# Kernel tuning notes

Hardware: AMD Instinct MI355X
Metric: run time of the kernel (lower is better)

Reference implementation:

```python
import jax, jax.numpy as jnp
import numpy as np

D_MODEL = 1024
N_HEADS = 16
D_K = D_MODEL // N_HEADS  # 64
THETA = 10000.0
MAX_SEQ_LEN = 2048


def _rope_cache():
    k = jnp.arange(D_K // 2, dtype=jnp.float32)
    inv_freq = THETA ** (-2.0 * k / D_K)  # [P]
    pos = jnp.arange(MAX_SEQ_LEN, dtype=jnp.float32)
    angles = pos[:, None] * inv_freq[None, :]  # [max_seq_len, P]
    return jnp.cos(angles), jnp.sin(angles)


def _apply_rope(x, cos, sin):
    # x: [B, H, S, d_k]; cos/sin: [B, 1, S, d_k//2] (broadcast over heads)
    x_even = x[..., 0::2]
    x_odd = x[..., 1::2]
    r_even = x_even * cos - x_odd * sin
    r_odd = x_even * sin + x_odd * cos
    # re-interleave pairs: [..., P, 2] -> [..., d_k]
    return jnp.stack([r_even, r_odd], axis=-1).reshape(x.shape)


def setup_inputs() -> dict:
    key = jax.random.key(0)
    ks = jax.random.split(key, 6)
    B, S = 4, 2048
    in_features = jax.random.normal(ks[0], (B, S, D_MODEL), dtype=jnp.float32)
    token_positions = jnp.sort(
        jax.random.randint(ks[1], (B, S), 0, MAX_SEQ_LEN), axis=-1
    ).astype(jnp.int64)
    std = np.sqrt(2.0 / (D_MODEL + D_MODEL))
    Wq = jax.random.truncated_normal(ks[2], -3.0, 3.0, (D_MODEL, D_MODEL), jnp.float32) * std
    Wk = jax.random.truncated_normal(ks[3], -3.0, 3.0, (D_MODEL, D_MODEL), jnp.float32) * std
    Wv = jax.random.truncated_normal(ks[4], -3.0, 3.0, (D_MODEL, D_MODEL), jnp.float32) * std
    Wo = jax.random.truncated_normal(ks[5], -3.0, 3.0, (D_MODEL, D_MODEL), jnp.float32) * std
    return {"in_features": in_features, "token_positions": token_positions,
            "Wq": Wq, "Wk": Wk, "Wv": Wv, "Wo": Wo}


def reference(in_features, token_positions, Wq, Wk, Wv, Wo):
    B, S, D = in_features.shape
    # fused-style QKV projections (RJLinear: x @ W.T)
    Q = in_features @ Wq.T
    K = in_features @ Wk.T
    V = in_features @ Wv.T
    # [B, S, H*dk] -> [B, H, S, dk]
    def split_heads(t):
        return t.reshape(B, S, N_HEADS, D_K).transpose(0, 2, 1, 3)
    Q, K, V = split_heads(Q), split_heads(K), split_heads(V)
    # RoPE using precomputed cache, gathered by token positions
    cos_cache, sin_cache = _rope_cache()
    pos = token_positions  # [B, S]
    cos = cos_cache[pos][:, None, :, :]  # [B, 1, S, P]
    sin = sin_cache[pos][:, None, :, :]
    Q = _apply_rope(Q, cos, sin)
    K = _apply_rope(K, cos, sin)
    # causal scaled dot-product attention
    scale = 1.0 / jnp.sqrt(jnp.float32(D_K))
    scores = jnp.einsum("bhqd,bhkd->bhqk", Q, K) * scale
    causal = jnp.tril(jnp.ones((S, S), dtype=bool))
    scores = jnp.where(causal[None, None, :, :], scores, -jnp.inf)
    weights = jax.nn.softmax(scores, axis=-1)
    attn = jnp.einsum("bhqk,bhkd->bhqd", weights, V)  # [B, H, S, dk]
    attn = attn.transpose(0, 2, 1, 3).reshape(B, S, D)
    return attn @ Wo.T
```

## Files before the change

### kernel.cpp

```cpp
#include <hip/hip_runtime.h>
#include <hip/hip_bf16.h>

typedef __bf16 bf16;
typedef bf16 bf16x8 __attribute__((ext_vector_type(8)));
typedef bf16 bf16x4 __attribute__((ext_vector_type(4)));
typedef float f32x4 __attribute__((ext_vector_type(4)));
typedef float f32x16 __attribute__((ext_vector_type(16)));
typedef unsigned short ushortT;
typedef ushortT ushort8 __attribute__((ext_vector_type(8)));

#define DEV __device__ __forceinline__

constexpr int DMODEL = 1024;
constexpr int NH = 16;
constexpr int DK = 64;
constexpr int SEQ = 2048;
constexpr int BATCH = 4;
constexpr int MROWS = BATCH * SEQ;
constexpr int KDIM = 1024;

#define GLOAD_LDS16(g, l) __builtin_amdgcn_global_load_lds( \
    (const __attribute__((address_space(1))) void*)(g), \
    (__attribute__((address_space(3))) void*)(l), 16, 0, 0)

__global__ void cvt_bf16(const float* __restrict__ src, bf16* __restrict__ dst, int n) {
    int i = (blockIdx.x * blockDim.x + threadIdx.x) * 8;
    if (i >= n) return;
    float4 f0 = *reinterpret_cast<const float4*>(src + i);
    float4 f1 = *reinterpret_cast<const float4*>(src + i + 4);
    bf16x8 o;
    o[0] = (bf16)f0.x; o[1] = (bf16)f0.y; o[2] = (bf16)f0.z; o[3] = (bf16)f0.w;
    o[4] = (bf16)f1.x; o[5] = (bf16)f1.y; o[6] = (bf16)f1.z; o[7] = (bf16)f1.w;
    *reinterpret_cast<bf16x8*>(dst + i) = o;
}

__global__ void cvt_bf16_w(const float* __restrict__ s0, const float* __restrict__ s1,
                           const float* __restrict__ s2, const float* __restrict__ s3,
                           bf16* __restrict__ d0, bf16* __restrict__ d1,
                           bf16* __restrict__ d2, bf16* __restrict__ d3) {
    int which = blockIdx.y;
    const float* s = which == 0 ? s0 : which == 1 ? s1 : which == 2 ? s2 : s3;
    bf16* d = which == 0 ? d0 : which == 1 ? d1 : which == 2 ? d2 : d3;
    int i = (blockIdx.x * blockDim.x + threadIdx.x) * 8;
    float4 f0 = *reinterpret_cast<const float4*>(s + i);
    float4 f1 = *reinterpret_cast<const float4*>(s + i + 4);
    bf16x8 o;
    o[0] = (bf16)f0.x; o[1] = (bf16)f0.y; o[2] = (bf16)f0.z; o[3] = (bf16)f0.w;
    o[4] = (bf16)f1.x; o[5] = (bf16)f1.y; o[6] = (bf16)f1.z; o[7] = (bf16)f1.w;
    *reinterpret_cast<bf16x8*>(d + i) = o;
}

__global__ void rope_tab(float2* __restrict__ csT) {
    int i = blockIdx.x * blockDim.x + threadIdx.x;
    int p = i >> 5, k = i & 31;
    float inv = powf(10000.0f, -2.0f * (float)k / 64.0f);
    float ang = (float)p * inv;
    csT[i] = make_float2(cosf(ang), sinf(ang));
}

__global__ __launch_bounds__(256) void gemm_qkv(
    const bf16* __restrict__ Xb,
    const bf16* __restrict__ Wqb, const bf16* __restrict__ Wkb, const bf16* __restrict__ Wvb,
    bf16* __restrict__ Qb, bf16* __restrict__ Kb, bf16* __restrict__ Vb,
    const int* __restrict__ tokpos, const float2* __restrict__ csT)
{
    __shared__ bf16 As[128 * 64];
    __shared__ bf16 Bs[128 * 64];

    const int which = blockIdx.z;
    const bf16* Bmat = which == 0 ? Wqb : (which == 1 ? Wkb : Wvb);
    bf16* Out = which == 0 ? Qb : (which == 1 ? Kb : Vb);

    const int m0 = blockIdx.x * 128;
    const int n0 = blockIdx.y * 128;
    const int t = threadIdx.x;
    const int w = t >> 6, l = t & 63;
    const int wd = w >> 1, ws = w & 1;
    const int lrow = l >> 3;
    const int lcol = (l & 7) * 8;
    const int lm = l & 15, lg = l >> 4;

    f32x4 acc[4][4] = {};

    for (int kt = 0; kt < KDIM; kt += 64) {
#pragma unroll
        for (int c = 0; c < 4; ++c) {
            int ci = c * 4 + w;
            int row = ci * 8 + lrow;
            const bf16* ga = Xb + (size_t)(m0 + row) * KDIM + kt + lcol;
            const bf16* gb = Bmat + (size_t)(n0 + row) * KDIM + kt + lcol;
            GLOAD_LDS16(ga, As + ci * 512);
            GLOAD_LDS16(gb, Bs + ci * 512);
        }
        __syncthreads();
#pragma unroll
        for (int kk = 0; kk < 2; ++kk) {
            bf16x8 wf[4], xf[4];
#pragma unroll
            for (int ni = 0; ni < 4; ++ni)
                wf[ni] = *reinterpret_cast<const bf16x8*>(Bs + (wd * 64 + ni * 16 + lm) * 64 + kk * 32 + lg * 8);
#pragma unroll
            for (int mi = 0; mi < 4; ++mi)
                xf[mi] = *reinterpret_cast<const bf16x8*>(As + (ws * 64 + mi * 16 + lm) * 64 + kk * 32 + lg * 8);
#pragma unroll
            for (int ni = 0; ni < 4; ++ni)
#pragma unroll
                for (int mi = 0; mi < 4; ++mi)
                    acc[ni][mi] = __builtin_amdgcn_mfma_f32_16x16x32_bf16(wf[ni], xf[mi], acc[ni][mi], 0, 0, 0);
        }
        __syncthreads();
    }

    const int h = (int)blockIdx.y * 2 + wd;
#pragma unroll
    for (int mi = 0; mi < 4; ++mi) {
        const int rowg = m0 + ws * 64 + mi * 16 + lm;
        const int b = rowg >> 11, ss = rowg & 2047;
        const size_t obase = ((size_t)(b * NH + h) * SEQ + ss) * DK;
        int p = 0;
        if (which < 2) p = tokpos[rowg];
#pragma unroll
        for (int ni = 0; ni < 4; ++ni) {
            const int dloc = ni * 16 + lg * 4;
            f32x4 a = acc[ni][mi];
            bf16x4 v4;
            if (which < 2) {
                const int k2 = dloc >> 1;
                float2 cs0 = csT[p * 32 + k2];
                float2 cs1 = csT[p * 32 + k2 + 1];
                v4[0] = (bf16)(a[0] * cs0.x - a[1] * cs0.y);
                v4[1] = (bf16)(a[0] * cs0.y + a[1] * cs0.x);
                v4[2] = (bf16)(a[2] * cs1.x - a[3] * cs1.y);
                v4[3] = (bf16)(a[2] * cs1.y + a[3] * cs1.x);
            } else {
                v4[0] = (bf16)a[0]; v4[1] = (bf16)a[1];
                v4[2] = (bf16)a[2]; v4[3] = (bf16)a[3];
            }
            *reinterpret_cast<bf16x4*>(Out + obase + dloc) = v4;
        }
    }
}

__global__ void vtrans(const bf16* __restrict__ Vb, bf16* __restrict__ Vt) {
    __shared__ ushortT tile[64][66];
    int bh = blockIdx.y, st = blockIdx.x;
    int t = threadIdx.x;
    int r = t >> 2, c4 = (t & 3) * 16;
    const ushortT* src = (const ushortT*)(Vb + ((size_t)bh * SEQ + st * 64 + r) * DK + c4);
    *reinterpret_cast<ushort8*>(&tile[r][c4]) = *reinterpret_cast<const ushort8*>(src);
    *reinterpret_cast<ushort8*>(&tile[r][c4 + 8]) = *reinterpret_cast<const ushort8*>(src + 8);
    __syncthreads();
    ushortT a[16];
#pragma unroll
    for (int i = 0; i < 16; ++i) a[i] = tile[c4 + i][r];
    ushort8 n0, n1;
#pragma unroll
    for (int i = 0; i < 4; ++i) {
        n0[i] = a[i];       n0[4 + i] = a[8 + i];
        n1[i] = a[4 + i];   n1[4 + i] = a[12 + i];
    }
    ushortT* dst = (ushortT*)(Vt + ((size_t)bh * DK + r) * SEQ + st * 64 + c4);
    *reinterpret_cast<ushort8*>(dst) = n0;
    *reinterpret_cast<ushort8*>(dst + 8) = n1;
}

constexpr float CL = 0.18033688011112042f;
constexpr float THR = 64.0f;

template<int MODE>
DEV void tileproc(const bf16* __restrict__ Klb, const bf16* __restrict__ Vlb,
                  int kv0, int q_abs, int ql, int hi, int swq,
                  const bf16x8 qb[4], f32x16 o[2], float& lsum, float& mrow)
{
    f32x16 s0 = {}, s1 = {};
#pragma unroll
    for (int sl = 0; sl < 4; ++sl) {
        bf16x8 k0 = *reinterpret_cast<const bf16x8*>(&Klb[ql * 64 + (((sl * 2 + hi) ^ swq) * 8)]);
        s0 = __builtin_amdgcn_mfma_f32_32x32x16_bf16(k0, qb[sl], s0, 0, 0, 0);
        if (MODE != 2) {
            bf16x8 k1 = *reinterpret_cast<const bf16x8*>(&Klb[(32 + ql) * 64 + (((sl * 2 + hi) ^ swq) * 8)]);
            s1 = __builtin_amdgcn_mfma_f32_32x32x16_bf16(k1, qb[sl], s1, 0, 0, 0);
        }
    }

    if (MODE >= 1) {
#pragma unroll
        for (int r = 0; r < 16; ++r) {
            const int kvl = (r & 3) + 8 * (r >> 2) + 4 * hi;
            if (kv0 + kvl > q_abs) s0[r] = -1e30f;
            if (MODE == 1 && kv0 + 32 + kvl > q_abs) s1[r] = -1e30f;
        }
    }

    f32x16 mm = s0;
    if (MODE != 2) {
#pragma unroll
        for (int r = 0; r < 16; ++r) mm[r] = fmaxf(mm[r], s1[r]);
    }
    float m0 = fmaxf(fmaxf(mm[0], mm[1]), fmaxf(mm[2], mm[3]));
    float m1 = fmaxf(fmaxf(mm[4], mm[5]), fmaxf(mm[6], mm[7]));
    float m2 = fmaxf(fmaxf(mm[8], mm[9]), fmaxf(mm[10], mm[11]));
    float m3 = fmaxf(fmaxf(mm[12], mm[13]), fmaxf(mm[14], mm[15]));
    float pmax = fmaxf(fmaxf(m0, m1), fmaxf(m2, m3));
    pmax = fmaxf(pmax, __shfl_xor(pmax, 32));

    if (!__all(pmax <= mrow + THR)) {
        const float mnew = fmaxf(mrow, pmax);
        const float alpha = __builtin_amdgcn_exp2f((mrow - mnew) * CL);
        mrow = mnew;
        lsum *= alpha;
        o[0] *= alpha;
        o[1] *= alpha;
    }

#pragma unroll
    for (int r = 0; r < 16; ++r) {
        s0[r] = __builtin_amdgcn_exp2f((s0[r] - mrow) * CL);
        if (MODE != 2) s1[r] = __builtin_amdgcn_exp2f((s1[r] - mrow) * CL);
    }
    {
        float a0 = (s0[0] + s0[1]) + (s0[2] + s0[3]);
        float a1 = (s0[4] + s0[5]) + (s0[6] + s0[7]);
        float a2 = (s0[8] + s0[9]) + (s0[10] + s0[11]);
        float a3 = (s0[12] + s0[13]) + (s0[14] + s0[15]);
        float ps = (a0 + a1) + (a2 + a3);
        if (MODE != 2) {
            float b0 = (s1[0] + s1[1]) + (s1[2] + s1[3]);
            float b1 = (s1[4] + s1[5]) + (s1[6] + s1[7]);
            float b2 = (s1[8] + s1[9]) + (s1[10] + s1[11]);
            float b3 = (s1[12] + s1[13]) + (s1[14] + s1[15]);
            ps += (b0 + b1) + (b2 + b3);
        }
        lsum += ps;
    }

#pragma unroll
    for (int c = 0; c < (MODE == 2 ? 1 : 2); ++c) {
#pragma unroll
        for (int u2 = 0; u2 < 2; ++u2) {
            const int u = c * 2 + u2;
            bf16x8 pb;
#pragma unroll
            for (int j = 0; j < 8; ++j) pb[j] = (bf16)(c ? s1[u2 * 8 + j] : s0[u2 * 8 + j]);
#pragma unroll
            for (int dt = 0; dt < 2; ++dt) {
                bf16x8 va = *reinterpret_cast<const bf16x8*>(
                    &Vlb[(dt * 32 + ql) * 64 + (((u * 2 + hi) ^ swq) * 8)]);
                o[dt] = __builtin_amdgcn_mfma_f32_32x32x16_bf16(va, pb, o[dt], 0, 0, 0);
            }
        }
    }
}

__global__ __launch_bounds__(256, 3) void attn(
    const bf16* __restrict__ Qb, const bf16* __restrict__ Kb, const bf16* __restrict__ Vt,
    bf16* __restrict__ Ab)
{
    __shared__ bf16 Kl[2][64 * 64];
    __shared__ bf16 Vl[2][64 * 64];

    const int bh = blockIdx.x;
    const int qt = (int)gridDim.y - 1 - (int)blockIdx.y;
    const int t = threadIdx.x, w = t >> 6, l = t & 63;
    const int ql = l & 31, hi = l >> 5;
    const int q0 = qt * 128 + w * 32;
    const bf16* Qh = Qb + (size_t)bh * SEQ * DK;
    const bf16* Kh = Kb + (size_t)bh * SEQ * DK;
    const bf16* Vh = Vt + (size_t)bh * DK * SEQ;

    const int lr = l >> 3, slot = l & 7;
    const int sw8 = ((slot ^ lr) * 8);
    const int r0 = w * 8 + lr;

    auto stage = [&](int tile, int buf) {
        const int kv0 = tile * 64;
        GLOAD_LDS16(Kh + (size_t)(kv0 + r0) * DK + sw8,       &Kl[buf][w * 512]);
        GLOAD_LDS16(Kh + (size_t)(kv0 + 32 + r0) * DK + sw8,  &Kl[buf][2048 + w * 512]);
        GLOAD_LDS16(Vh + (size_t)r0 * SEQ + kv0 + sw8,        &Vl[buf][w * 512]);
        GLOAD_LDS16(Vh + (size_t)(32 + r0) * SEQ + kv0 + sw8, &Vl[buf][2048 + w * 512]);
    };

    bf16x8 qb[4];
#pragma unroll
    for (int sl = 0; sl < 4; ++sl)
        qb[sl] = *reinterpret_cast<const bf16x8*>(Qh + (size_t)(q0 + ql) * DK + sl * 16 + hi * 8);

    f32x16 o[2] = {};
    float lsum = 0.0f;
    float mrow = -1e30f;
    const int q_abs = q0 + ql;
    const int swq = ql & 7;

    const int ntile = 2 * qt + 2;
    stage(0, 0);
    __syncthreads();
    for (int tt = 0; tt < ntile; ++tt) {
        if (tt + 1 < ntile) stage(tt + 1, (tt + 1) & 1);
        const int kv0 = tt * 64;
        const bf16* Klb = &Kl[tt & 1][0];
        const bf16* Vlb = &Vl[tt & 1][0];
        if (tt < 2 * qt) {
            tileproc<0>(Klb, Vlb, kv0, q_abs, ql, hi, swq, qb, o, lsum, mrow);
        } else {
            const bool a0 = kv0 <= q0 + 31;
            const bool a1 = kv0 + 32 <= q0 + 31;
            if (a1)      tileproc<1>(Klb, Vlb, kv0, q_abs, ql, hi, swq, qb, o, lsum, mrow);
            else if (a0) tileproc<2>(Klb, Vlb, kv0, q_abs, ql, hi, swq, qb, o, lsum, mrow);
        }
        __syncthreads();
    }

    const float rs = lsum + __shfl_xor(lsum, 32);
    const float rinv = 1.0f / rs;

    const int b = bh >> 4, h = bh & 15;
    const int q = q0 + ql;
    const size_t rowbase = ((size_t)(b * SEQ + q)) * DMODEL + h * 64;
#pragma unroll
    for (int dt = 0; dt < 2; ++dt)
#pragma unroll
        for (int g = 0; g < 4; ++g) {
            bf16x4 v4;
#pragma unroll
            for (int e = 0; e < 4; ++e) v4[e] = (bf16)(o[dt][4 * g + e] * rinv);
            *reinterpret_cast<bf16x4*>(Ab + rowbase + dt * 32 + 8 * g + 4 * hi) = v4;
        }
}

__global__ __launch_bounds__(256) void gemm_out(
    const bf16* __restrict__ Ab, const bf16* __restrict__ Wob, float* __restrict__ Out)
{
    __shared__ bf16 As[128 * 64];
    __shared__ bf16 Bs[128 * 64];

    const int m0 = blockIdx.x * 128;
    const int n0 = blockIdx.y * 128;
    const int t = threadIdx.x;
    const int w = t >> 6, l = t & 63;
    const int wd = w >> 1, ws = w & 1;
    const int lrow = l >> 3;
    const int lcol = (l & 7) * 8;
    const int lm = l & 15, lg = l >> 4;

    f32x4 acc[4][4] = {};

    for (int kt = 0; kt < KDIM; kt += 64) {
#pragma unroll
        for (int c = 0; c < 4; ++c) {
            int ci = c * 4 + w;
            int row = ci * 8 + lrow;
            const bf16* ga = Ab + (size_t)(m0 + row) * KDIM + kt + lcol;
            const bf16* gb = Wob + (size_t)(n0 + row) * KDIM + kt + lcol;
            GLOAD_LDS16(ga, As + ci * 512);
            GLOAD_LDS16(gb, Bs + ci * 512);
        }
        __syncthreads();
#pragma unroll
        for (int kk = 0; kk < 2; ++kk) {
            bf16x8 wf[4], xf[4];
#pragma unroll
            for (int ni = 0; ni < 4; ++ni)
                wf[ni] = *reinterpret_cast<const bf16x8*>(Bs + (wd * 64 + ni * 16 + lm) * 64 + kk * 32 + lg * 8);
#pragma unroll
            for (int mi = 0; mi < 4; ++mi)
                xf[mi] = *reinterpret_cast<const bf16x8*>(As + (ws * 64 + mi * 16 + lm) * 64 + kk * 32 + lg * 8);
#pragma unroll
            for (int ni = 0; ni < 4; ++ni)
#pragma unroll
                for (int mi = 0; mi < 4; ++mi)
                    acc[ni][mi] = __builtin_amdgcn_mfma_f32_16x16x32_bf16(wf[ni], xf[mi], acc[ni][mi], 0, 0, 0);
        }
        __syncthreads();
    }

#pragma unroll
    for (int mi = 0; mi < 4; ++mi) {
        const int rowg = m0 + ws * 64 + mi * 16 + lm;
#pragma unroll
        for (int ni = 0; ni < 4; ++ni) {
            const int ncol = n0 + wd * 64 + ni * 16 + lg * 4;
            *reinterpret_cast<f32x4*>(Out + (size_t)rowg * DMODEL + ncol) = acc[ni][mi];
        }
    }
}

extern "C" void kernel_launch(void* const* d_in, const int* in_sizes, int n_in,
                              void* d_out, int out_size, void* d_ws, size_t ws_size,
                              hipStream_t stream) {
    const float* X  = (const float*)d_in[0];
    const int* tokpos = (const int*)d_in[1];
    const float* Wq = (const float*)d_in[2];
    const float* Wk = (const float*)d_in[3];
    const float* Wv = (const float*)d_in[4];
    const float* Wo = (const float*)d_in[5];

    char* ws = (char*)d_ws;
    bf16* Xb  = (bf16*)(ws + 0);
    bf16* Wqb = (bf16*)(ws + 16777216);
    bf16* Wkb = (bf16*)(ws + 18874368);
    bf16* Wvb = (bf16*)(ws + 20971520);
    bf16* Wob = (bf16*)(ws + 23068672);
    float2* csT = (float2*)(ws + 25165824);
    bf16* Qb = (bf16*)(ws + 25690112);
    bf16* Kb = (bf16*)(ws + 42467328);
    bf16* Vb = (bf16*)(ws + 59244544);
    bf16* Vt = (bf16*)(ws + 76021760);
    bf16* Ab = (bf16*)(ws + 92798976);

    cvt_bf16<<<4096, 256, 0, stream>>>(X, Xb, MROWS * DMODEL);
    cvt_bf16_w<<<dim3(512, 4), 256, 0, stream>>>(Wq, Wk, Wv, Wo, Wqb, Wkb, Wvb, Wob);
    rope_tab<<<256, 256, 0, stream>>>(csT);

    gemm_qkv<<<dim3(MROWS / 128, DMODEL / 128, 3), 256, 0, stream>>>(
        Xb, Wqb, Wkb, Wvb, Qb, Kb, Vb, tokpos, csT);

    vtrans<<<dim3(SEQ / 64, BATCH * NH), 256, 0, stream>>>(Vb, Vt);

    attn<<<dim3(BATCH * NH, SEQ / 128), 256, 0, stream>>>(Qb, Kb, Vt, Ab);

    gemm_out<<<dim3(MROWS / 128, DMODEL / 128), 256, 0, stream>>>(Ab, Wob, (float*)d_out);
}
```

Baseline: 203.1 us.

## Pipeline QKV and output GEMMs with 4-stage LDS ring and XOR swizzle

Measured after the change: 201.1 us. About the same (-1.0%).

```diff
diff --git a/kernel.cpp b/kernel.cpp
--- a/kernel.cpp
+++ b/kernel.cpp
@@ -22,6 +22,13 @@
 #define GLOAD_LDS16(g, l) __builtin_amdgcn_global_load_lds( \
     (const __attribute__((address_space(1))) void*)(g), \
     (__attribute__((address_space(3))) void*)(l), 16, 0, 0)
+
+#define PIPE_WAIT(N) do { \
+    __builtin_amdgcn_sched_barrier(0); \
+    asm volatile("s_waitcnt vmcnt(" #N ")" ::: "memory"); \
+    __builtin_amdgcn_s_barrier(); \
+    __builtin_amdgcn_sched_barrier(0); \
+} while (0)
 
 __global__ void cvt_bf16(const float* __restrict__ src, bf16* __restrict__ dst, int n) {
     int i = (blockIdx.x * blockDim.x + threadIdx.x) * 8;
@@ -64,8 +71,8 @@
     bf16* __restrict__ Qb, bf16* __restrict__ Kb, bf16* __restrict__ Vb,
     const int* __restrict__ tokpos, const float2* __restrict__ csT)
 {
-    __shared__ bf16 As[128 * 64];
-    __shared__ bf16 Bs[128 * 64];
+    __shared__ bf16 As[4][64 * 64];
+    __shared__ bf16 Bs[4][64 * 64];
 
     const int which = blockIdx.z;
     const bf16* Bmat = which == 0 ? Wqb : (which == 1 ? Wkb : Wvb);
@@ -76,40 +83,54 @@
     const int t = threadIdx.x;
     const int w = t >> 6, l = t & 63;
     const int wd = w >> 1, ws = w & 1;
-    const int lrow = l >> 3;
-    const int lcol = (l & 7) * 8;
     const int lm = l & 15, lg = l >> 4;
+    const int lr = l >> 3, sE = l & 7;
+    const int lgc = sE ^ lr;
+    const int trO = lr + ((lgc >> 2) << 6);
+    const int kO = (lgc & 3) * 8;
+    const int slA = (((ws * 4 + lg) ^ (lm & 7)) * 8);
+    const int slB = (((wd * 4 + lg) ^ (lm & 7)) * 8);
 
     f32x4 acc[4][4] = {};
 
-    for (int kt = 0; kt < KDIM; kt += 64) {
-#pragma unroll
-        for (int c = 0; c < 4; ++c) {
-            int ci = c * 4 + w;
-            int row = ci * 8 + lrow;
-            const bf16* ga = Xb + (size_t)(m0 + row) * KDIM + kt + lcol;
-            const bf16* gb = Bmat + (size_t)(n0 + row) * KDIM + kt + lcol;
-            GLOAD_LDS16(ga, As + ci * 512);
-            GLOAD_LDS16(gb, Bs + ci * 512);
-        }
-        __syncthreads();
-#pragma unroll
-        for (int kk = 0; kk < 2; ++kk) {
-            bf16x8 wf[4], xf[4];
-#pragma unroll
-            for (int ni = 0; ni < 4; ++ni)
-                wf[ni] = *reinterpret_cast<const bf16x8*>(Bs + (wd * 64 + ni * 16 + lm) * 64 + kk * 32 + lg * 8);
+    auto stage = [&](int kt, int kb) {
+#pragma unroll
+        for (int c = 0; c < 2; ++c) {
+            const int ci = c * 4 + w;
+            GLOAD_LDS16(Xb + (size_t)(m0 + ci * 8 + trO) * KDIM + kt + kO, &As[kb][ci * 512]);
+            GLOAD_LDS16(Bmat + (size_t)(n0 + ci * 8 + trO) * KDIM + kt + kO, &Bs[kb][ci * 512]);
+        }
+    };
+
+    auto compute = [&](int kb) {
+        bf16x8 wf[4], xf[4];
+#pragma unroll
+        for (int ni = 0; ni < 4; ++ni)
+            wf[ni] = *reinterpret_cast<const bf16x8*>(&Bs[kb][(ni * 16 + lm) * 64 + slB]);
+#pragma unroll
+        for (int mi = 0; mi < 4; ++mi)
+            xf[mi] = *reinterpret_cast<const bf16x8*>(&As[kb][(mi * 16 + lm) * 64 + slA]);
+        __builtin_amdgcn_s_setprio(1);
+#pragma unroll
+        for (int ni = 0; ni < 4; ++ni)
 #pragma unroll
             for (int mi = 0; mi < 4; ++mi)
-                xf[mi] = *reinterpret_cast<const bf16x8*>(As + (ws * 64 + mi * 16 + lm) * 64 + kk * 32 + lg * 8);
-#pragma unroll
-            for (int ni = 0; ni < 4; ++ni)
-#pragma unroll
-                for (int mi = 0; mi < 4; ++mi)
-                    acc[ni][mi] = __builtin_amdgcn_mfma_f32_16x16x32_bf16(wf[ni], xf[mi], acc[ni][mi], 0, 0, 0);
-        }
-        __syncthreads();
-    }
+                acc[ni][mi] = __builtin_amdgcn_mfma_f32_16x16x32_bf16(wf[ni], xf[mi], acc[ni][mi], 0, 0, 0);
+        __builtin_amdgcn_s_setprio(0);
+    };
+
+    stage(0, 0);
+    stage(32, 1);
+    stage(64, 2);
+    PIPE_WAIT(8);
+    for (int it = 0; it < 29; ++it) {
+        stage(it * 32 + 96, (it + 3) & 3);
+        compute(it & 3);
+        PIPE_WAIT(8);
+    }
+    compute(1); PIPE_WAIT(4);
+    compute(2); PIPE_WAIT(0);
+    compute(3);
 
     const int h = (int)blockIdx.y * 2 + wd;
 #pragma unroll
@@ -330,48 +351,62 @@
 __global__ __launch_bounds__(256) void gemm_out(
     const bf16* __restrict__ Ab, const bf16* __restrict__ Wob, float* __restrict__ Out)
 {
-    __shared__ bf16 As[128 * 64];
-    __shared__ bf16 Bs[128 * 64];
+    __shared__ bf16 As[4][64 * 64];
+    __shared__ bf16 Bs[4][64 * 64];
 
     const int m0 = blockIdx.x * 128;
     const int n0 = blockIdx.y * 128;
     const int t = threadIdx.x;
     const int w = t >> 6, l = t & 63;
     const int wd = w >> 1, ws = w & 1;
-    const int lrow = l >> 3;
-    const int lcol = (l & 7) * 8;
     const int lm = l & 15, lg = l >> 4;
+    const int lr = l >> 3, sE = l & 7;
+    const int lgc = sE ^ lr;
+    const int trO = lr + ((lgc >> 2) << 6);
+    const int kO = (lgc & 3) * 8;
+    const int slA = (((ws * 4 + lg) ^ (lm & 7)) * 8);
+    const int slB = (((wd * 4 + lg) ^ (lm & 7)) * 8);
 
     f32x4 acc[4][4] = {};
 
-    for (int kt = 0; kt < KDIM; kt += 64) {
-#pragma unroll
-        for (int c = 0; c < 4; ++c) {
-            int ci = c * 4 + w;
-            int row = ci * 8 + lrow;
-            const bf16* ga = Ab + (size_t)(m0 + row) * KDIM + kt + lcol;
-            const bf16* gb = Wob + (size_t)(n0 + row) * KDIM + kt + lcol;
-            GLOAD_LDS16(ga, As + ci * 512);
-            GLOAD_LDS16(gb, Bs + ci * 512);
-        }
-        __syncthreads();
-#pragma unroll
-        for (int kk = 0; kk < 2; ++kk) {
-            bf16x8 wf[4], xf[4];
-#pragma unroll
-            for (int ni = 0; ni < 4; ++ni)
-                wf[ni] = *reinterpret_cast<const bf16x8*>(Bs + (wd * 64 + ni * 16 + lm) * 64 + kk * 32 + lg * 8);
+    auto stage = [&](int kt, int kb) {
+#pragma unroll
+        for (int c = 0; c < 2; ++c) {
+            const int ci = c * 4 + w;
+            GLOAD_LDS16(Ab + (size_t)(m0 + ci * 8 + trO) * KDIM + kt + kO, &As[kb][ci * 512]);
+            GLOAD_LDS16(Wob + (size_t)(n0 + ci * 8 + trO) * KDIM + kt + kO, &Bs[kb][ci * 512]);
+        }
+    };
+
+    auto compute = [&](int kb) {
+        bf16x8 wf[4], xf[4];
+#pragma unroll
+        for (int ni = 0; ni < 4; ++ni)
+            wf[ni] = *reinterpret_cast<const bf16x8*>(&Bs[kb][(ni * 16 + lm) * 64 + slB]);
+#pragma unroll
+        for (int mi = 0; mi < 4; ++mi)
+            xf[mi] = *reinterpret_cast<const bf16x8*>(&As[kb][(mi * 16 + lm) * 64 + slA]);
+        __builtin_amdgcn_s_setprio(1);
+#pragma unroll
+        for (int ni = 0; ni < 4; ++ni)
 #pragma unroll
             for (int mi = 0; mi < 4; ++mi)
-                xf[mi] = *reinterpret_cast<const bf16x8*>(As + (ws * 64 + mi * 16 + lm) * 64 + kk * 32 + lg * 8);
-#pragma unroll
-            for (int ni = 0; ni < 4; ++ni)
-#pragma unroll
-                for (int mi = 0; mi < 4; ++mi)
-                    acc[ni][mi] = __builtin_amdgcn_mfma_f32_16x16x32_bf16(wf[ni], xf[mi], acc[ni][mi], 0, 0, 0);
-        }
-        __syncthreads();
-    }
+                acc[ni][mi] = __builtin_amdgcn_mfma_f32_16x16x32_bf16(wf[ni], xf[mi], acc[ni][mi], 0, 0, 0);
+        __builtin_amdgcn_s_setprio(0);
+    };
+
+    stage(0, 0);
+    stage(32, 1);
+    stage(64, 2);
+    PIPE_WAIT(8);
+    for (int it = 0; it < 29; ++it) {
+        stage(it * 32 + 96, (it + 3) & 3);
+        compute(it & 3);
+        PIPE_WAIT(8);
+    }
+    compute(1); PIPE_WAIT(4);
+    compute(2); PIPE_WAIT(0);
+    compute(3);
 
 #pragma unroll
     for (int mi = 0; mi < 4; ++mi) {
```
